# Kernel tuning notes

Measured on AMD Instinct MI355X. Metric: run time of the kernel, lower is better.

## Reference

```python
import jax, jax.numpy as jnp
import numpy as np

N_NODES = 100000
N_EDGES = 1600000
D_IN = 128
D_HID = 128


def setup_inputs() -> dict:
    key = jax.random.key(0)
    ks = jax.random.split(key, 8)
    scale_in = 1.0 / np.sqrt(D_IN)
    scale_h = 1.0 / np.sqrt(D_HID)
    return {
        "x": jax.random.normal(ks[0], (N_NODES, D_IN), dtype=jnp.float32),
        "edge_index": jax.random.randint(ks[1], (2, N_EDGES), 0, N_NODES, dtype=jnp.int64),
        "W_l1": jax.random.normal(ks[2], (D_IN, D_HID), dtype=jnp.float32) * scale_in,
        "W_r1": jax.random.normal(ks[3], (D_IN, D_HID), dtype=jnp.float32) * scale_in,
        "b1": jnp.zeros((D_HID,), dtype=jnp.float32),
        "W_l2": jax.random.normal(ks[4], (D_HID, D_HID), dtype=jnp.float32) * scale_h,
        "W_r2": jax.random.normal(ks[5], (D_HID, D_HID), dtype=jnp.float32) * scale_h,
        "b2": jnp.zeros((D_HID,), dtype=jnp.float32),
    }


def _sage_conv(h, src, dst, n_nodes, W_l, W_r, b):
    # mean aggregation of source-node features onto destination nodes
    msg = h[src]                                         # [E, d] gather
    agg = jax.ops.segment_sum(msg, dst, num_segments=n_nodes)   # [N, d]
    cnt = jax.ops.segment_sum(jnp.ones((src.shape[0], 1), h.dtype), dst,
                              num_segments=n_nodes)      # [N, 1]
    mean = agg / jnp.maximum(cnt, 1.0)                   # zero where no in-edges
    return mean @ W_l + b + h @ W_r                      # lin_l(mean) + lin_r(x)


def reference(x, edge_index, W_l1, W_r1, b1, W_l2, W_r2, b2):
    src, dst = edge_index[0], edge_index[1]
    n = x.shape[0]
    h = jax.nn.relu(_sage_conv(x, src, dst, n, W_l1, W_r1, b1))
    # dropout is identity in eval mode
    return _sage_conv(h, src, dst, n, W_l2, W_r2, b2)
```

## Files before the change

### kernel.cpp

```cpp
#include <hip/hip_runtime.h>
#include <stdint.h>

#define N_NODES 100000
#define N_EDGES 1600000
#define D 128
#define NBUCK 196
#define BSTRIDE 9216
#define PCHUNK 2048
#define NTILES (N_NODES / 16)
#define GRID_AG 2048

typedef unsigned int uint32;
typedef __attribute__((ext_vector_type(8))) short short8;
typedef __attribute__((ext_vector_type(4))) float f32x4;

__device__ __forceinline__ unsigned short f2bf(float f) {
  unsigned u = __builtin_bit_cast(unsigned, f);
  u += 0x7fffu + ((u >> 16) & 1u);
  return (unsigned short)(u >> 16);
}
__device__ __forceinline__ float bflo(unsigned v) {
  return __builtin_bit_cast(float, v << 16);
}
__device__ __forceinline__ float bfhi(unsigned v) {
  return __builtin_bit_cast(float, v & 0xffff0000u);
}


__global__ __launch_bounds__(256) void k_part(const int* __restrict__ src,
                                              const int* __restrict__ dst,
                                              int* __restrict__ bcnt,
                                              uint2* __restrict__ pairs) {
  __shared__ uint2 buff[PCHUNK];
  __shared__ uint2 sorted[PCHUNK];
  __shared__ int hist[256], stmp[256], loff[256], cpos[256], base[256];
  int tid = threadIdx.x;
  int e0 = blockIdx.x * PCHUNK;
  int nv = N_EDGES - e0;
  if (nv > PCHUNK) nv = PCHUNK;

  hist[tid] = 0;
  __syncthreads();
  for (int i = tid; i < nv; i += 256) {
    int d = dst[e0 + i];
    int s = src[e0 + i];
    buff[i] = make_uint2((uint32)d, (uint32)s);
    atomicAdd(&hist[d >> 9], 1);
  }
  __syncthreads();
  int v = hist[tid];
  stmp[tid] = v;
  __syncthreads();
  for (int off = 1; off < 256; off <<= 1) {
    int t = (tid >= off) ? stmp[tid - off] : 0;
    __syncthreads();
    stmp[tid] += t;
    __syncthreads();
  }
  loff[tid] = stmp[tid] - v;
  cpos[tid] = stmp[tid] - v;
  base[tid] = (v > 0) ? atomicAdd(&bcnt[tid], v) : 0;
  __syncthreads();
  for (int i = tid; i < nv; i += 256) {
    uint2 p = buff[i];
    int r = atomicAdd(&cpos[p.x >> 9], 1);
    sorted[r] = p;
  }
  __syncthreads();
  for (int i = tid; i < nv; i += 256) {
    uint2 p = sorted[i];
    int b = (int)(p.x >> 9);
    int local = base[b] + (i - loff[b]);
    if (local < BSTRIDE)
      pairs[(size_t)b * BSTRIDE + local] = p;
  }
}

__global__ void k_scanb(const int* __restrict__ bcnt, int* __restrict__ bbase) {
  __shared__ int s[256];
  int tid = threadIdx.x;
  int v = (tid < NBUCK) ? bcnt[tid] : 0;
  s[tid] = v;
  __syncthreads();
  for (int off = 1; off < 256; off <<= 1) {
    int t = (tid >= off) ? s[tid - off] : 0;
    __syncthreads();
    s[tid] += t;
    __syncthreads();
  }
  if (tid <= NBUCK) bbase[tid] = s[tid] - v;
}

__global__ __launch_bounds__(512) void k_csr(const uint2* __restrict__ pairs,
                                             const int* __restrict__ bcnt,
                                             const int* __restrict__ bbase,
                                             int* __restrict__ rowptr,
                                             int* __restrict__ csr) {
  __shared__ int hist[512], off[512], cur[512];
  int b = blockIdx.x;
  int tid = threadIdx.x;
  int lo = b << 9;
  int hi = lo + 512;
  if (hi > N_NODES) hi = N_NODES;
  int ne = bcnt[b];
  if (ne > BSTRIDE) ne = BSTRIDE;
  const uint2* pb = pairs + (size_t)b * BSTRIDE;
  int bb = bbase[b];

  hist[tid] = 0;
  __syncthreads();
  for (int i = tid; i < ne; i += 512) atomicAdd(&hist[(int)pb[i].x - lo], 1);
  __syncthreads();
  int v = hist[tid];
  off[tid] = v;
  __syncthreads();
  for (int o = 1; o < 512; o <<= 1) {
    int t = (tid >= o) ? off[tid - o] : 0;
    __syncthreads();
    off[tid] += t;
    __syncthreads();
  }
  off[tid] -= v;
  cur[tid] = off[tid];
  if (lo + tid < hi) rowptr[lo + tid] = bb + off[tid];
  if (b == NBUCK - 1 && tid == 0) rowptr[N_NODES] = bbase[NBUCK];
  __syncthreads();
  for (int i = tid; i < ne; i += 512) {
    int d = (int)pb[i].x - lo;
    int slot = atomicAdd(&cur[d], 1);
    csr[bb + slot] = (int)pb[i].y;
  }
}


__global__ void k_cast(const float* __restrict__ in, unsigned short* __restrict__ ob, int n8) {
  int i = blockIdx.x * blockDim.x + threadIdx.x;
  if (i >= n8) return;
  float4 a = *reinterpret_cast<const float4*>(in + (size_t)i * 8);
  float4 b = *reinterpret_cast<const float4*>(in + (size_t)i * 8 + 4);
  uint4 o;
  o.x = (uint32)f2bf(a.x) | ((uint32)f2bf(a.y) << 16);
  o.y = (uint32)f2bf(a.z) | ((uint32)f2bf(a.w) << 16);
  o.z = (uint32)f2bf(b.x) | ((uint32)f2bf(b.y) << 16);
  o.w = (uint32)f2bf(b.z) | ((uint32)f2bf(b.w) << 16);
  *reinterpret_cast<uint4*>(ob + (size_t)i * 8) = o;
}

__global__ void k_prepw2(const float* __restrict__ Wl1, const float* __restrict__ Wr1,
                         const float* __restrict__ Wl2, const float* __restrict__ Wr2,
                         unsigned short* __restrict__ Wp1,
                         unsigned short* __restrict__ Wp2) {
  int t = blockIdx.x * 256 + threadIdx.x;
  int which = t >> 15;
  int tt = t & 32767;
  int j = tt & 7;
  int lane = (tt >> 3) & 63;
  int tile = (tt >> 9) & 1;
  int ks = (tt >> 10) & 7;
  int ng = (tt >> 13) & 3;
  int k = ks * 32 + (lane >> 4) * 8 + j;
  int n = ng * 32 + tile * 16 + (lane & 15);
  const float* Wl = which ? Wl2 : Wl1;
  const float* Wr = which ? Wr2 : Wr1;
  float w = (k < 128) ? Wl[k * 128 + n] : Wr[(k - 128) * 128 + n];
  (which ? Wp2 : Wp1)[tt] = f2bf(w);
}

#define ACC8(v)                                          \
  acc[0] += bflo(v.x); acc[1] += bfhi(v.x);              \
  acc[2] += bflo(v.y); acc[3] += bfhi(v.y);              \
  acc[4] += bflo(v.z); acc[5] += bfhi(v.z);              \
  acc[6] += bflo(v.w); acc[7] += bfhi(v.w);

__global__ __launch_bounds__(256) void k_agg_gemm(
    const unsigned short* __restrict__ table,
    const int* __restrict__ rowptr, const int* __restrict__ csr,
    const unsigned short* __restrict__ Wp, const float* __restrict__ bias,
    void* __restrict__ outp, int relu_bf16_out) {
  __shared__ float meanS[16][132];
  int tid = threadIdx.x;
  int wave = tid >> 6;
  int lane = tid & 63;
  int q = lane >> 4;
  int r = lane & 15;
  int g = tid >> 4;
  int l = tid & 15;

  short8 Bf[8][2];
  const unsigned short* wp = Wp + ((size_t)wave * 8 * 2) * 64 * 8 + lane * 8;
#pragma unroll
  for (int ks = 0; ks < 8; ++ks)
#pragma unroll
    for (int t = 0; t < 2; ++t)
      Bf[ks][t] = *reinterpret_cast<const short8*>(wp + (ks * 2 + t) * 512);

  float bia0 = bias[wave * 32 + r];
  float bia1 = bias[wave * 32 + 16 + r];

  for (int tile = blockIdx.x; tile < NTILES; tile += GRID_AG) {
    const unsigned short* ax = table + (size_t)(tile * 16 + r) * D + q * 8;
    short8 A[8];
#pragma unroll
    for (int ks = 0; ks < 4; ++ks)
      A[4 + ks] = *reinterpret_cast<const short8*>(ax + ks * 32);

    int node = tile * 16 + g;
    int beg = rowptr[node], end = rowptr[node + 1];
    float acc[8] = {0.f, 0.f, 0.f, 0.f, 0.f, 0.f, 0.f, 0.f};
    int e = beg;
    for (; e + 3 < end; e += 4) {
      int s0 = csr[e], s1 = csr[e + 1], s2 = csr[e + 2], s3 = csr[e + 3];
      uint4 v0 = *reinterpret_cast<const uint4*>(table + (size_t)s0 * D + l * 8);
      uint4 v1 = *reinterpret_cast<const uint4*>(table + (size_t)s1 * D + l * 8);
      uint4 v2 = *reinterpret_cast<const uint4*>(table + (size_t)s2 * D + l * 8);
      uint4 v3 = *reinterpret_cast<const uint4*>(table + (size_t)s3 * D + l * 8);
      ACC8(v0) ACC8(v1) ACC8(v2) ACC8(v3)
    }
    for (; e < end; ++e) {
      int s0 = csr[e];
      uint4 v0 = *reinterpret_cast<const uint4*>(table + (size_t)s0 * D + l * 8);
      ACC8(v0)
    }
    float inv = (end > beg) ? 1.0f / (float)(end - beg) : 0.0f;
    float4 m0 = make_float4(acc[0] * inv, acc[1] * inv, acc[2] * inv, acc[3] * inv);
    float4 m1 = make_float4(acc[4] * inv, acc[5] * inv, acc[6] * inv, acc[7] * inv);
    *reinterpret_cast<float4*>(&meanS[g][l * 8]) = m0;
    *reinterpret_cast<float4*>(&meanS[g][l * 8 + 4]) = m1;
    __syncthreads();

#pragma unroll
    for (int ks = 0; ks < 4; ++ks) {
      float4 a0 = *reinterpret_cast<const float4*>(&meanS[r][ks * 32 + q * 8]);
      float4 a1 = *reinterpret_cast<const float4*>(&meanS[r][ks * 32 + q * 8 + 4]);
      short8 a;
      a[0] = (short)f2bf(a0.x); a[1] = (short)f2bf(a0.y);
      a[2] = (short)f2bf(a0.z); a[3] = (short)f2bf(a0.w);
      a[4] = (short)f2bf(a1.x); a[5] = (short)f2bf(a1.y);
      a[6] = (short)f2bf(a1.z); a[7] = (short)f2bf(a1.w);
      A[ks] = a;
    }

    f32x4 c0 = {0.f, 0.f, 0.f, 0.f}, c1 = {0.f, 0.f, 0.f, 0.f};
#pragma unroll
    for (int ks = 0; ks < 8; ++ks) {
      c0 = __builtin_amdgcn_mfma_f32_16x16x32_bf16(A[ks], Bf[ks][0], c0, 0, 0, 0);
      c1 = __builtin_amdgcn_mfma_f32_16x16x32_bf16(A[ks], Bf[ks][1], c1, 0, 0, 0);
    }

    int orow = tile * 16 + q * 4;
    if (relu_bf16_out) {
      unsigned short* ob = (unsigned short*)outp + (size_t)orow * D + wave * 32 + r;
#pragma unroll
      for (int gg = 0; gg < 4; ++gg) {
        ob[(size_t)gg * D] = f2bf(fmaxf(c0[gg] + bia0, 0.f));
        ob[(size_t)gg * D + 16] = f2bf(fmaxf(c1[gg] + bia1, 0.f));
      }
    } else {
      float* of = (float*)outp + (size_t)orow * D + wave * 32 + r;
#pragma unroll
      for (int gg = 0; gg < 4; ++gg) {
        of[(size_t)gg * D] = c0[gg] + bia0;
        of[(size_t)gg * D + 16] = c1[gg] + bia1;
      }
    }
    __syncthreads();
  }
}


extern "C" void kernel_launch(void* const* d_in, const int* in_sizes, int n_in,
                              void* d_out, int out_size, void* d_ws, size_t ws_size,
                              hipStream_t stream) {
  const float* x   = (const float*)d_in[0];
  const int*   ei  = (const int*)d_in[1];
  const float* Wl1 = (const float*)d_in[2];
  const float* Wr1 = (const float*)d_in[3];
  const float* b1  = (const float*)d_in[4];
  const float* Wl2 = (const float*)d_in[5];
  const float* Wr2 = (const float*)d_in[6];
  const float* b2  = (const float*)d_in[7];
  float* out = (float*)d_out;

  const int* esrc = ei;
  const int* edst = ei + N_EDGES;

  char* p = (char*)d_ws;
  auto take = [&](size_t bytes) {
    char* q = p;
    p += (bytes + 255) & ~(size_t)255;
    return q;
  };
  int* bcnt   = (int*)take(256 * 4);
  int* bbase  = (int*)take(257 * 4);
  int* rowptr = (int*)take((size_t)(N_NODES + 1) * 4);
  int* csr    = (int*)take((size_t)N_EDGES * 4);
  uint2* pairs = (uint2*)take((size_t)NBUCK * BSTRIDE * 8);
  unsigned short* xb  = (unsigned short*)take((size_t)N_NODES * D * 2);
  unsigned short* hb  = (unsigned short*)take((size_t)N_NODES * D * 2);
  unsigned short* Wp1 = (unsigned short*)take(256 * 128 * 2);
  unsigned short* Wp2 = (unsigned short*)take(256 * 128 * 2);

  const int npart = (N_EDGES + PCHUNK - 1) / PCHUNK;

  hipMemsetAsync(bcnt, 0, 256 * 4, stream);
  k_part<<<npart, 256, 0, stream>>>(esrc, edst, bcnt, pairs);
  k_scanb<<<1, 256, 0, stream>>>(bcnt, bbase);
  k_csr<<<NBUCK, 512, 0, stream>>>(pairs, bcnt, bbase, rowptr, csr);

  k_cast<<<(N_NODES * D / 8 + 255) / 256, 256, 0, stream>>>(x, xb, N_NODES * D / 8);
  k_prepw2<<<256, 256, 0, stream>>>(Wl1, Wr1, Wl2, Wr2, Wp1, Wp2);

  k_agg_gemm<<<GRID_AG, 256, 0, stream>>>(xb, rowptr, csr, Wp1, b1, hb, 1);
  k_agg_gemm<<<GRID_AG, 256, 0, stream>>>(hb, rowptr, csr, Wp2, b2, out, 0);
}
```

Measured before the change: 330.3 us.

## Balance edge aggregation across thread groups with LDS atomics per tile

Each 16-node tile's edge range is now split evenly across the 16 thread groups instead of giving each group one node, so threads no longer wait on high-degree nodes. Partial sums are added into the shared mean buffer with LDS atomics whenever a group's slice crosses a node boundary, and the division by degree is moved to the point where the mean buffer is converted to bf16. This adds a zeroing pass, an extra barrier, boundary bookkeeping and atomic contention on nodes shared between groups.

After: 538.0 us. 62.9% more time.

```diff
diff --git a/kernel.cpp b/kernel.cpp
--- a/kernel.cpp
+++ b/kernel.cpp
@@ -178,6 +178,7 @@
     const unsigned short* __restrict__ Wp, const float* __restrict__ bias,
     void* __restrict__ outp, int relu_bf16_out) {
   __shared__ float meanS[16][132];
+  __shared__ int bnd[17];
   int tid = threadIdx.x;
   int wave = tid >> 6;
   int lane = tid & 63;
@@ -198,45 +199,71 @@
   float bia1 = bias[wave * 32 + 16 + r];
 
   for (int tile = blockIdx.x; tile < NTILES; tile += GRID_AG) {
-    const unsigned short* ax = table + (size_t)(tile * 16 + r) * D + q * 8;
+    int t16 = tile * 16;
+    const unsigned short* ax = table + (size_t)(t16 + r) * D + q * 8;
     short8 A[8];
 #pragma unroll
     for (int ks = 0; ks < 4; ++ks)
       A[4 + ks] = *reinterpret_cast<const short8*>(ax + ks * 32);
 
-    int node = tile * 16 + g;
-    int beg = rowptr[node], end = rowptr[node + 1];
-    float acc[8] = {0.f, 0.f, 0.f, 0.f, 0.f, 0.f, 0.f, 0.f};
-    int e = beg;
-    for (; e + 3 < end; e += 4) {
-      int s0 = csr[e], s1 = csr[e + 1], s2 = csr[e + 2], s3 = csr[e + 3];
-      uint4 v0 = *reinterpret_cast<const uint4*>(table + (size_t)s0 * D + l * 8);
-      uint4 v1 = *reinterpret_cast<const uint4*>(table + (size_t)s1 * D + l * 8);
-      uint4 v2 = *reinterpret_cast<const uint4*>(table + (size_t)s2 * D + l * 8);
-      uint4 v3 = *reinterpret_cast<const uint4*>(table + (size_t)s3 * D + l * 8);
-      ACC8(v0) ACC8(v1) ACC8(v2) ACC8(v3)
-    }
-    for (; e < end; ++e) {
-      int s0 = csr[e];
-      uint4 v0 = *reinterpret_cast<const uint4*>(table + (size_t)s0 * D + l * 8);
-      ACC8(v0)
-    }
-    float inv = (end > beg) ? 1.0f / (float)(end - beg) : 0.0f;
-    float4 m0 = make_float4(acc[0] * inv, acc[1] * inv, acc[2] * inv, acc[3] * inv);
-    float4 m1 = make_float4(acc[4] * inv, acc[5] * inv, acc[6] * inv, acc[7] * inv);
-    *reinterpret_cast<float4*>(&meanS[g][l * 8]) = m0;
-    *reinterpret_cast<float4*>(&meanS[g][l * 8 + 4]) = m1;
-    __syncthreads();
-
+    if (tid < 17) bnd[tid] = rowptr[t16 + tid];
+    {
+      float4 z = make_float4(0.f, 0.f, 0.f, 0.f);
+      *reinterpret_cast<float4*>(&meanS[g][l * 8]) = z;
+      *reinterpret_cast<float4*>(&meanS[g][l * 8 + 4]) = z;
+    }
+    __syncthreads();
+
+    int eb = bnd[0], ee = bnd[16];
+    int nE = ee - eb;
+    int per = (nE + 15) >> 4;
+    int s = eb + g * per;
+    int sEnd = s + per;
+    if (sEnd > ee) sEnd = ee;
+    if (s < sEnd) {
+      int cn = 0;
+      while (s >= bnd[cn + 1]) ++cn;
+      float acc[8] = {0.f, 0.f, 0.f, 0.f, 0.f, 0.f, 0.f, 0.f};
+      int e = s;
+      while (e < sEnd) {
+        int nodeEnd = bnd[cn + 1];
+        int lim = nodeEnd < sEnd ? nodeEnd : sEnd;
+        int segStart = e;
+        for (; e + 3 < lim; e += 4) {
+          int s0 = csr[e], s1 = csr[e + 1], s2 = csr[e + 2], s3 = csr[e + 3];
+          uint4 v0 = *reinterpret_cast<const uint4*>(table + (size_t)s0 * D + l * 8);
+          uint4 v1 = *reinterpret_cast<const uint4*>(table + (size_t)s1 * D + l * 8);
+          uint4 v2 = *reinterpret_cast<const uint4*>(table + (size_t)s2 * D + l * 8);
+          uint4 v3 = *reinterpret_cast<const uint4*>(table + (size_t)s3 * D + l * 8);
+          ACC8(v0) ACC8(v1) ACC8(v2) ACC8(v3)
+        }
+        for (; e < lim; ++e) {
+          int s0 = csr[e];
+          uint4 v0 = *reinterpret_cast<const uint4*>(table + (size_t)s0 * D + l * 8);
+          ACC8(v0)
+        }
+        if (e > segStart) {
+#pragma unroll
+          for (int j = 0; j < 8; ++j) atomicAdd(&meanS[cn][l * 8 + j], acc[j]);
+#pragma unroll
+          for (int j = 0; j < 8; ++j) acc[j] = 0.f;
+        }
+        if (lim == nodeEnd) ++cn;
+      }
+    }
+    __syncthreads();
+
+    int deg = bnd[r + 1] - bnd[r];
+    float inv = (deg > 0) ? 1.0f / (float)deg : 0.0f;
 #pragma unroll
     for (int ks = 0; ks < 4; ++ks) {
       float4 a0 = *reinterpret_cast<const float4*>(&meanS[r][ks * 32 + q * 8]);
       float4 a1 = *reinterpret_cast<const float4*>(&meanS[r][ks * 32 + q * 8 + 4]);
       short8 a;
-      a[0] = (short)f2bf(a0.x); a[1] = (short)f2bf(a0.y);
-      a[2] = (short)f2bf(a0.z); a[3] = (short)f2bf(a0.w);
-      a[4] = (short)f2bf(a1.x); a[5] = (short)f2bf(a1.y);
-      a[6] = (short)f2bf(a1.z); a[7] = (short)f2bf(a1.w);
+      a[0] = (short)f2bf(a0.x * inv); a[1] = (short)f2bf(a0.y * inv);
+      a[2] = (short)f2bf(a0.z * inv); a[3] = (short)f2bf(a0.w * inv);
+      a[4] = (short)f2bf(a1.x * inv); a[5] = (short)f2bf(a1.y * inv);
+      a[6] = (short)f2bf(a1.z * inv); a[7] = (short)f2bf(a1.w * inv);
       A[ks] = a;
     }
 
@@ -247,7 +274,7 @@
       c1 = __builtin_amdgcn_mfma_f32_16x16x32_bf16(A[ks], Bf[ks][1], c1, 0, 0, 0);
     }
 
-    int orow = tile * 16 + q * 4;
+    int orow = t16 + q * 4;
     if (relu_bf16_out) {
       unsigned short* ob = (unsigned short*)outp + (size_t)orow * D + wave * 32 + r;
 #pragma unroll
```
